# Performance work log

Hardware: AMD Instinct MI355X
Metric: run time of the kernel (lower is better)

Reference implementation:

```python
import jax, jax.numpy as jnp
import numpy as np

B, N, DIM = 4, 2048, 1024
H, DH = 16, 64
SCALE = DH ** -0.5


def setup_inputs() -> dict:
    key = jax.random.key(0)
    k1, k2, k3, k4 = jax.random.split(key, 4)
    x = jax.random.normal(k1, (B, N, DIM), dtype=jnp.float32)
    mask = jax.random.randint(k2, (B, N, N), 0, 2, dtype=jnp.int32)
    W_qkv = jax.random.normal(k3, (DIM, 3 * H * DH), dtype=jnp.float32) * (DIM ** -0.5)
    W_out = jax.random.normal(k4, (H * DH, DIM), dtype=jnp.float32) * ((H * DH) ** -0.5)
    b_out = jnp.zeros((DIM,), dtype=jnp.float32)
    return {"x": x, "mask": mask, "W_qkv": W_qkv, "W_out": W_out, "b_out": b_out}


def reference(x, mask, W_qkv, W_out, b_out):
    # QKV projection: [b, n, 3*h*d]
    qkv = x @ W_qkv
    q, k, v = jnp.split(qkv, 3, axis=-1)
    # 'b n (h d) -> b h n d'
    def to_heads(t):
        b, n, _ = t.shape
        return t.reshape(b, n, H, DH).transpose(0, 2, 1, 3)
    q, k, v = to_heads(q), to_heads(k), to_heads(v)
    # scaled dot-product scores: [b, h, n, n]
    scores = jnp.einsum('bhnd,bhmd->bhnm', q, k) * SCALE
    scores = jnp.where(mask[:, None, :, :] == 1, -jnp.inf, scores)
    att = jax.nn.softmax(scores, axis=-1)
    out = jnp.einsum('bhnm,bhmd->bhnd', att, v)
    # 'b h n d -> b n (h d)'
    out = out.transpose(0, 2, 1, 3).reshape(x.shape[0], x.shape[1], H * DH)
    return out @ W_out + b_out
```

## Files before the change

kernel.cpp:

```cpp
#include <hip/hip_runtime.h>
#include <hip/hip_bf16.h>


typedef __attribute__((ext_vector_type(8))) short bf16x8;
typedef __attribute__((ext_vector_type(4))) float f32x4;

__device__ __forceinline__ unsigned short f2bf(float f) {
  unsigned u = __builtin_bit_cast(unsigned, f);
  u += 0x7fffu + ((u >> 16) & 1u);
  return (unsigned short)(u >> 16);
}

__device__ __forceinline__ void gload16(const void* g, void* l) {
  __builtin_amdgcn_global_load_lds(
      (const __attribute__((address_space(1))) unsigned int*)g,
      (__attribute__((address_space(3))) unsigned int*)l, 16, 0, 0);
}

__device__ __forceinline__ bf16x8 ldsw(const short* base, int row, int elem) {
  const char* p = (const char*)base + row * 128 + ((elem * 2) ^ ((row & 7) << 4));
  return *(const bf16x8*)p;
}

__global__ __launch_bounds__(256) void k_cvt(const float* __restrict__ in,
                                             unsigned short* __restrict__ out) {
  int i = (blockIdx.x * 256 + threadIdx.x) * 4;
  float4 v = *reinterpret_cast<const float4*>(in + i);
  ushort4 o;
  o.x = f2bf(v.x); o.y = f2bf(v.y); o.z = f2bf(v.z); o.w = f2bf(v.w);
  *reinterpret_cast<ushort4*>(out + i) = o;
}

__global__ __launch_bounds__(256) void k_transpose_cvt(const float* __restrict__ in,
                                                       unsigned short* __restrict__ out,
                                                       int rows, int cols) {
  __shared__ float tile[32][33];
  int tx = threadIdx.x & 31, ty = threadIdx.x >> 5;
  int c0 = blockIdx.x * 32, r0 = blockIdx.y * 32;
#pragma unroll
  for (int i = 0; i < 32; i += 8)
    tile[ty + i][tx] = in[(size_t)(r0 + ty + i) * cols + (c0 + tx)];
  __syncthreads();
#pragma unroll
  for (int i = 0; i < 32; i += 8)
    out[(size_t)(c0 + ty + i) * rows + (r0 + tx)] = f2bf(tile[tx][ty + i]);
}

__global__ __launch_bounds__(256) void k_packmask(const int* __restrict__ mask,
                                                  unsigned long long* __restrict__ pack) {
  const int row = blockIdx.x;
  const int t = threadIdx.x, w = t >> 6, lane = t & 63;
  const int* mrow = mask + (size_t)row * 2048;
#pragma unroll
  for (int it = 0; it < 8; ++it) {
    int key = it * 256 + w * 64 + lane;
    unsigned long long bal = __ballot(mrow[key] == 1);
    if (lane == 0) pack[(size_t)row * 32 + it * 4 + w] = bal;
  }
}

template <int EPI>
__global__ __launch_bounds__(256) void k_gemm(
    const unsigned short* __restrict__ A, const unsigned short* __restrict__ Bt,
    unsigned short* __restrict__ Qo, unsigned short* __restrict__ Ko,
    unsigned short* __restrict__ Vo, float* __restrict__ Co,
    const float* __restrict__ bias) {
  __shared__ __align__(16) short Smem[16896];
  short* As = Smem;
  short* Bs = Smem + 8192;
  const int t = threadIdx.x;
  const int NBN = (EPI == 0) ? 24 : 8;
  const int orig = blockIdx.y * NBN + blockIdx.x;
  const int wgid = (orig & 7) * (NBN * 8) + (orig >> 3);
  const int bn = wgid % NBN, bm = wgid / NBN;
  const int wid = t >> 6, lane = t & 63, g = lane >> 4, l15 = lane & 15;
  const int wr = wid >> 1, wc = wid & 1;
  f32x4 zero = {0.f, 0.f, 0.f, 0.f};
  f32x4 acc[4][4];
#pragma unroll
  for (int i = 0; i < 4; ++i)
#pragma unroll
    for (int j = 0; j < 4; ++j) acc[i][j] = zero;

  const char* Ab = (const char*)(A + (size_t)bm * 128 * 1024);
  const char* Bb = (const char*)(Bt + (size_t)bn * 128 * 1024);

  for (int k0 = 0; k0 < 2048; k0 += 128) {
#pragma unroll
    for (int q = 0; q < 4; ++q) {
      int idx = t + q * 256, r = idx >> 3, c = idx & 7;
      int sw = (c * 16) ^ ((r & 7) << 4);
      gload16(Ab + (size_t)r * 2048 + k0 + sw, (char*)As + idx * 16);
      gload16(Bb + (size_t)r * 2048 + k0 + sw, (char*)Bs + idx * 16);
    }
    asm volatile("s_waitcnt vmcnt(0)" ::: "memory");
    __syncthreads();
#pragma unroll
    for (int ks = 0; ks < 2; ++ks) {
      bf16x8 a[4], b[4];
#pragma unroll
      for (int mi = 0; mi < 4; ++mi) a[mi] = ldsw(As, wr * 64 + mi * 16 + l15, ks * 32 + g * 8);
#pragma unroll
      for (int ni = 0; ni < 4; ++ni) b[ni] = ldsw(Bs, wc * 64 + ni * 16 + l15, ks * 32 + g * 8);
#pragma unroll
      for (int mi = 0; mi < 4; ++mi)
#pragma unroll
        for (int ni = 0; ni < 4; ++ni)
          acc[mi][ni] = __builtin_amdgcn_mfma_f32_16x16x32_bf16(a[mi], b[ni], acc[mi][ni], 0, 0, 0);
    }
    __syncthreads();
  }

  if (EPI == 1) {
#pragma unroll
    for (int mi = 0; mi < 4; ++mi)
#pragma unroll
      for (int ni = 0; ni < 4; ++ni)
#pragma unroll
        for (int j = 0; j < 4; ++j) {
          int row = bm * 128 + wr * 64 + mi * 16 + g * 4 + j;
          int col = bn * 128 + wc * 64 + ni * 16 + l15;
          Co[(size_t)row * 1024 + col] = acc[mi][ni][j] + bias[col];
        }
    return;
  }

  const int s = bn >> 3;
  const int h0 = (bn & 7) * 2;
  const int bglob = (bm * 128) >> 11;
  const int n0 = (bm * 128) & 2047;

  if (s < 2) {
    const float qs = (s == 0) ? 0.18033688011112042f : 1.0f;
#pragma unroll
    for (int mi = 0; mi < 4; ++mi)
#pragma unroll
      for (int ni = 0; ni < 4; ++ni)
#pragma unroll
        for (int j = 0; j < 4; ++j)
          Smem[(wr * 64 + mi * 16 + g * 4 + j) * 132 + wc * 64 + ni * 16 + l15] =
              (short)f2bf(acc[mi][ni][j] * qs);
    __syncthreads();
    int r = t >> 1, hh = t & 1;
    unsigned short* dst = (s == 0 ? Qo : Ko) +
        (((size_t)(bglob * 16 + h0 + hh)) * 2048 + n0 + r) * 64;
    const short* src = Smem + r * 132 + hh * 64;
#pragma unroll
    for (int k = 0; k < 8; ++k) {
      uint2 a = *reinterpret_cast<const uint2*>(src + k * 8);
      uint2 b2 = *reinterpret_cast<const uint2*>(src + k * 8 + 4);
      uint4 w = {a.x, a.y, b2.x, b2.y};
      *reinterpret_cast<uint4*>(dst + k * 8) = w;
    }
  } else {
#pragma unroll
    for (int mi = 0; mi < 4; ++mi)
#pragma unroll
      for (int ni = 0; ni < 4; ++ni) {
        unsigned x0 = f2bf(acc[mi][ni][0]), x1 = f2bf(acc[mi][ni][1]);
        unsigned x2 = f2bf(acc[mi][ni][2]), x3 = f2bf(acc[mi][ni][3]);
        uint2 pk = {x0 | (x1 << 16), x2 | (x3 << 16)};
        int col = wc * 64 + ni * 16 + l15;
        int row = wr * 64 + mi * 16 + g * 4;
        *reinterpret_cast<uint2*>(Smem + col * 132 + row) = pk;
      }
    __syncthreads();
    int c = t >> 1, seg = t & 1;
    int h = h0 + (c >> 6), d = c & 63;
    unsigned short* dst = Vo + ((size_t)(bglob * 16 + h) * 64 + d) * 2048 + n0 + seg * 64;
    const short* src = Smem + c * 132 + seg * 64;
#pragma unroll
    for (int k = 0; k < 8; ++k) {
      uint2 a = *reinterpret_cast<const uint2*>(src + k * 8);
      uint2 b2 = *reinterpret_cast<const uint2*>(src + k * 8 + 4);
      uint4 w = {a.x, a.y, b2.x, b2.y};
      *reinterpret_cast<uint4*>(dst + k * 8) = w;
    }
  }
}

__global__ __launch_bounds__(512, 8) void k_attn(
    const unsigned short* __restrict__ Q, const unsigned short* __restrict__ K,
    const unsigned short* __restrict__ Vt_g, const unsigned long long* __restrict__ pack,
    unsigned short* __restrict__ O) {
  __shared__ __align__(16) short Ks[2][64 * 64];
  __shared__ __align__(16) short Vt[2][64 * 64];
  __shared__ __align__(16) short Ps[8][16 * 32];
  const int bid0 = blockIdx.x;
  const int bid = (bid0 & 7) * 128 + (bid0 >> 3);
  const int qt = bid & 15, bh = bid >> 4;
  const int b = bh >> 4;
  const int t = threadIdx.x, wid = t >> 6, lane = t & 63, g = lane >> 4, l15 = lane & 15;
  const char* Kb = (const char*)(K + (size_t)bh * (2048 * 64));
  const char* Vb = (const char*)(Vt_g + (size_t)bh * (64 * 2048));
  const unsigned short* Qb = Q + (size_t)bh * (2048 * 64);

  const int sr = t >> 3, sc = t & 7;
  const int sw_src = (sc * 16) ^ ((sr & 7) << 4);
  char* PwB = (char*)&Ps[wid][0];
  const int ps_rd  = (l15 * 64 + g * 16) ^ ((l15 & 7) << 4);
  const int ps_wr0 = (l15 * 64 + g * 8) ^ ((l15 & 7) << 4);

  gload16(Kb + (size_t)sr * 128 + sw_src, (char*)&Ks[0][0] + t * 16);
  gload16(Vb + (size_t)sr * 4096 + sw_src, (char*)&Vt[0][0] + t * 16);
  const int qrow = qt * 128 + wid * 16 + l15;
  bf16x8 qf0 = *reinterpret_cast<const bf16x8*>(Qb + (size_t)qrow * 64 + g * 8);
  bf16x8 qf1 = *reinterpret_cast<const bf16x8*>(Qb + (size_t)qrow * 64 + 32 + g * 8);
  const unsigned long long* mrow = pack + ((size_t)b * 2048 + qrow) * 32;
  asm volatile("s_waitcnt vmcnt(0)" ::: "memory");
  __syncthreads();

  f32x4 zero = {0.f, 0.f, 0.f, 0.f};
  f32x4 oacc[4];
#pragma unroll
  for (int nf = 0; nf < 4; ++nf) oacc[nf] = zero;
  float lp = 0.f;

  int cb = 0;
#pragma unroll 1
  for (int kt = 0; kt < 32; ++kt) {
    const int nb = cb ^ 1;
    unsigned long long mw = mrow[kt];
    if (kt + 1 < 32) {
      gload16(Kb + (size_t)((kt + 1) * 64 + sr) * 128 + sw_src, (char*)&Ks[nb][0] + t * 16);
      gload16(Vb + (size_t)sr * 4096 + (kt + 1) * 128 + sw_src, (char*)&Vt[nb][0] + t * 16);
    }
    unsigned mlo = (unsigned)mw >> (g * 4);
    unsigned mhi = (unsigned)(mw >> 32) >> (g * 4);
#pragma unroll
    for (int kh = 0; kh < 2; ++kh) {
      f32x4 sf[2] = {zero, zero};
      __builtin_amdgcn_s_setprio(1);
#pragma unroll
      for (int ds = 0; ds < 2; ++ds) {
        bf16x8 qk = ds ? qf1 : qf0;
#pragma unroll
        for (int nf2 = 0; nf2 < 2; ++nf2) {
          bf16x8 kk = ldsw(&Ks[cb][0], (kh * 2 + nf2) * 16 + l15, ds * 32 + g * 8);
          sf[nf2] = __builtin_amdgcn_mfma_f32_16x16x32_bf16(kk, qk, sf[nf2], 0, 0, 0);
        }
      }
      __builtin_amdgcn_s_setprio(0);
      unsigned msrc = kh ? mhi : mlo;
#pragma unroll
      for (int nf2 = 0; nf2 < 2; ++nf2) {
        unsigned eu[4];
#pragma unroll
        for (int j = 0; j < 4; ++j) {
          float s = sf[nf2][j];
          if (msrc & (1u << (nf2 * 16 + j))) s = -1e30f;
          float e = __builtin_amdgcn_exp2f(s);
          lp += e;
          eu[j] = __builtin_bit_cast(unsigned, e);
        }
        uint2 pk;
        pk.x = __builtin_amdgcn_perm(eu[1], eu[0], 0x07060302);
        pk.y = __builtin_amdgcn_perm(eu[3], eu[2], 0x07060302);
        *reinterpret_cast<uint2*>(PwB + (nf2 ? (ps_wr0 ^ 32) : ps_wr0)) = pk;
      }
      asm volatile("s_waitcnt lgkmcnt(0)" ::: "memory");
      __builtin_amdgcn_sched_barrier(0);
      bf16x8 ap = *reinterpret_cast<const bf16x8*>(PwB + ps_rd);
      __builtin_amdgcn_s_setprio(1);
#pragma unroll
      for (int nf = 0; nf < 4; ++nf) {
        bf16x8 bv = ldsw(&Vt[cb][0], nf * 16 + l15, kh * 32 + g * 8);
        oacc[nf] = __builtin_amdgcn_mfma_f32_16x16x32_bf16(ap, bv, oacc[nf], 0, 0, 0);
      }
      __builtin_amdgcn_s_setprio(0);
    }
    asm volatile("s_waitcnt vmcnt(0)" ::: "memory");
    __syncthreads();
    cb = nb;
  }

  float l = lp;
  l += __shfl_xor(l, 16);
  l += __shfl_xor(l, 32);
  float invl = 1.0f / l;
  float inv[4];
#pragma unroll
  for (int j = 0; j < 4; ++j) inv[j] = __shfl(invl, g * 4 + j);

  const int h = bh & 15;
#pragma unroll
  for (int nf = 0; nf < 4; ++nf) {
#pragma unroll
    for (int j = 0; j < 4; ++j) {
      int qg = qt * 128 + wid * 16 + g * 4 + j;
      int d = nf * 16 + l15;
      O[((size_t)b * 2048 + qg) * 1024 + h * 64 + d] = f2bf(oacc[nf][j] * inv[j]);
    }
  }
}

extern "C" void kernel_launch(void* const* d_in, const int* in_sizes, int n_in,
                              void* d_out, int out_size, void* d_ws, size_t ws_size,
                              hipStream_t stream) {
  (void)in_sizes; (void)n_in; (void)out_size; (void)ws_size;
  const float* x = (const float*)d_in[0];
  const int* mask = (const int*)d_in[1];
  const float* Wqkv = (const float*)d_in[2];
  const float* Wout = (const float*)d_in[3];
  const float* bout = (const float*)d_in[4];
  float* out = (float*)d_out;

  unsigned short* ws = (unsigned short*)d_ws;
  unsigned short* Xb   = ws;
  unsigned short* Wq_t = Xb + 8388608;
  unsigned short* Wo_t = Wq_t + 3145728;
  unsigned short* Qa   = Wo_t + 1048576;
  unsigned short* Ka   = Qa + 8388608;
  unsigned short* Va   = Ka + 8388608;
  unsigned short* ATT  = Va + 8388608;
  unsigned long long* MP = (unsigned long long*)(ATT + 8388608);

  k_cvt<<<8192, 256, 0, stream>>>(x, Xb);
  k_transpose_cvt<<<dim3(96, 32), 256, 0, stream>>>(Wqkv, Wq_t, 1024, 3072);
  k_transpose_cvt<<<dim3(32, 32), 256, 0, stream>>>(Wout, Wo_t, 1024, 1024);
  k_packmask<<<8192, 256, 0, stream>>>(mask, MP);
  k_gemm<0><<<dim3(24, 64), 256, 0, stream>>>(Xb, Wq_t, Qa, Ka, Va, nullptr, nullptr);
  k_attn<<<1024, 512, 0, stream>>>(Qa, Ka, Va, MP, ATT);
  k_gemm<1><<<dim3(8, 64), 256, 0, stream>>>(ATT, Wo_t, nullptr, nullptr, nullptr, out, bout);
}
```

Before: 250.5 us.

## Use 32x32x16 MFMA in attention with permlane32 swap instead of LDS P staging

Attention now runs 4 waves of 256 threads per block, each wave owning 32 query rows, and uses 32x32x16 bf16 MFMAs for both QK^T and PV. The score tile is repacked into the PV A-operand layout with permlane32_swap, which removes the per-wave LDS round trip and its waitcnt. The GEMM's grouped block-index swizzle is also removed in favor of plain blockIdx mapping. Each block has fewer waves and more registers per thread, which could lower latency hiding, and dropping the swizzle may hurt L2 locality in the GEMMs.

```diff
diff --git a/kernel.cpp b/kernel.cpp
--- a/kernel.cpp
+++ b/kernel.cpp
@@ -4,6 +4,8 @@
 
 typedef __attribute__((ext_vector_type(8))) short bf16x8;
 typedef __attribute__((ext_vector_type(4))) float f32x4;
+typedef __attribute__((ext_vector_type(16))) float f32x16;
+typedef __attribute__((ext_vector_type(2))) unsigned int uint2v;
 
 __device__ __forceinline__ unsigned short f2bf(float f) {
   unsigned u = __builtin_bit_cast(unsigned, f);
@@ -69,10 +71,7 @@
   short* As = Smem;
   short* Bs = Smem + 8192;
   const int t = threadIdx.x;
-  const int NBN = (EPI == 0) ? 24 : 8;
-  const int orig = blockIdx.y * NBN + blockIdx.x;
-  const int wgid = (orig & 7) * (NBN * 8) + (orig >> 3);
-  const int bn = wgid % NBN, bm = wgid / NBN;
+  const int bn = blockIdx.x, bm = blockIdx.y;
   const int wid = t >> 6, lane = t & 63, g = lane >> 4, l15 = lane & 15;
   const int wr = wid >> 1, wc = wid & 1;
   f32x4 zero = {0.f, 0.f, 0.f, 0.f};
@@ -179,41 +178,45 @@
   }
 }
 
-__global__ __launch_bounds__(512, 8) void k_attn(
+__global__ __launch_bounds__(256) void k_attn(
     const unsigned short* __restrict__ Q, const unsigned short* __restrict__ K,
     const unsigned short* __restrict__ Vt_g, const unsigned long long* __restrict__ pack,
     unsigned short* __restrict__ O) {
   __shared__ __align__(16) short Ks[2][64 * 64];
   __shared__ __align__(16) short Vt[2][64 * 64];
-  __shared__ __align__(16) short Ps[8][16 * 32];
   const int bid0 = blockIdx.x;
   const int bid = (bid0 & 7) * 128 + (bid0 >> 3);
   const int qt = bid & 15, bh = bid >> 4;
   const int b = bh >> 4;
-  const int t = threadIdx.x, wid = t >> 6, lane = t & 63, g = lane >> 4, l15 = lane & 15;
+  const int t = threadIdx.x, wid = t >> 6, lane = t & 63;
+  const int l31 = lane & 31, hi = lane >> 5;
   const char* Kb = (const char*)(K + (size_t)bh * (2048 * 64));
   const char* Vb = (const char*)(Vt_g + (size_t)bh * (64 * 2048));
   const unsigned short* Qb = Q + (size_t)bh * (2048 * 64);
 
-  const int sr = t >> 3, sc = t & 7;
-  const int sw_src = (sc * 16) ^ ((sr & 7) << 4);
-  char* PwB = (char*)&Ps[wid][0];
-  const int ps_rd  = (l15 * 64 + g * 16) ^ ((l15 & 7) << 4);
-  const int ps_wr0 = (l15 * 64 + g * 8) ^ ((l15 & 7) << 4);
-
-  gload16(Kb + (size_t)sr * 128 + sw_src, (char*)&Ks[0][0] + t * 16);
-  gload16(Vb + (size_t)sr * 4096 + sw_src, (char*)&Vt[0][0] + t * 16);
-  const int qrow = qt * 128 + wid * 16 + l15;
-  bf16x8 qf0 = *reinterpret_cast<const bf16x8*>(Qb + (size_t)qrow * 64 + g * 8);
-  bf16x8 qf1 = *reinterpret_cast<const bf16x8*>(Qb + (size_t)qrow * 64 + 32 + g * 8);
+  const int i0 = t, i1 = t + 256;
+  const int r0s = i0 >> 3, r1s = i1 >> 3, cs = (t & 7) * 16;
+  const int k0off = r0s * 128 + (cs ^ ((r0s & 7) << 4));
+  const int k1off = r1s * 128 + (cs ^ ((r1s & 7) << 4));
+  const int v0off = r0s * 4096 + (cs ^ ((r0s & 7) << 4));
+  const int v1off = r1s * 4096 + (cs ^ ((r1s & 7) << 4));
+
+  gload16(Kb + k0off, (char*)&Ks[0][0] + i0 * 16);
+  gload16(Kb + k1off, (char*)&Ks[0][0] + i1 * 16);
+  gload16(Vb + v0off, (char*)&Vt[0][0] + i0 * 16);
+  gload16(Vb + v1off, (char*)&Vt[0][0] + i1 * 16);
+
+  const int qrow = qt * 128 + wid * 32 + l31;
+  bf16x8 qf[4];
+#pragma unroll
+  for (int c = 0; c < 4; ++c)
+    qf[c] = *reinterpret_cast<const bf16x8*>(Qb + (size_t)qrow * 64 + c * 16 + hi * 8);
   const unsigned long long* mrow = pack + ((size_t)b * 2048 + qrow) * 32;
   asm volatile("s_waitcnt vmcnt(0)" ::: "memory");
   __syncthreads();
 
-  f32x4 zero = {0.f, 0.f, 0.f, 0.f};
-  f32x4 oacc[4];
-#pragma unroll
-  for (int nf = 0; nf < 4; ++nf) oacc[nf] = zero;
+  f32x16 oacc0 = {0.f,0.f,0.f,0.f,0.f,0.f,0.f,0.f,0.f,0.f,0.f,0.f,0.f,0.f,0.f,0.f};
+  f32x16 oacc1 = {0.f,0.f,0.f,0.f,0.f,0.f,0.f,0.f,0.f,0.f,0.f,0.f,0.f,0.f,0.f,0.f};
   float lp = 0.f;
 
   int cb = 0;
@@ -222,50 +225,55 @@
     const int nb = cb ^ 1;
     unsigned long long mw = mrow[kt];
     if (kt + 1 < 32) {
-      gload16(Kb + (size_t)((kt + 1) * 64 + sr) * 128 + sw_src, (char*)&Ks[nb][0] + t * 16);
-      gload16(Vb + (size_t)sr * 4096 + (kt + 1) * 128 + sw_src, (char*)&Vt[nb][0] + t * 16);
-    }
-    unsigned mlo = (unsigned)mw >> (g * 4);
-    unsigned mhi = (unsigned)(mw >> 32) >> (g * 4);
+      gload16(Kb + (kt + 1) * 8192 + k0off, (char*)&Ks[nb][0] + i0 * 16);
+      gload16(Kb + (kt + 1) * 8192 + k1off, (char*)&Ks[nb][0] + i1 * 16);
+      gload16(Vb + (kt + 1) * 128 + v0off, (char*)&Vt[nb][0] + i0 * 16);
+      gload16(Vb + (kt + 1) * 128 + v1off, (char*)&Vt[nb][0] + i1 * 16);
+    }
 #pragma unroll
     for (int kh = 0; kh < 2; ++kh) {
-      f32x4 sf[2] = {zero, zero};
+      unsigned m32 = (unsigned)(kh ? (mw >> 32) : mw) >> (4 * hi);
+      f32x16 sf = {0.f,0.f,0.f,0.f,0.f,0.f,0.f,0.f,0.f,0.f,0.f,0.f,0.f,0.f,0.f,0.f};
       __builtin_amdgcn_s_setprio(1);
 #pragma unroll
-      for (int ds = 0; ds < 2; ++ds) {
-        bf16x8 qk = ds ? qf1 : qf0;
-#pragma unroll
-        for (int nf2 = 0; nf2 < 2; ++nf2) {
-          bf16x8 kk = ldsw(&Ks[cb][0], (kh * 2 + nf2) * 16 + l15, ds * 32 + g * 8);
-          sf[nf2] = __builtin_amdgcn_mfma_f32_16x16x32_bf16(kk, qk, sf[nf2], 0, 0, 0);
-        }
+      for (int c = 0; c < 4; ++c) {
+        bf16x8 kk = ldsw(&Ks[cb][0], kh * 32 + l31, c * 16 + hi * 8);
+        sf = __builtin_amdgcn_mfma_f32_32x32x16_bf16(kk, qf[c], sf, 0, 0, 0);
       }
       __builtin_amdgcn_s_setprio(0);
-      unsigned msrc = kh ? mhi : mlo;
-#pragma unroll
-      for (int nf2 = 0; nf2 < 2; ++nf2) {
-        unsigned eu[4];
-#pragma unroll
-        for (int j = 0; j < 4; ++j) {
-          float s = sf[nf2][j];
-          if (msrc & (1u << (nf2 * 16 + j))) s = -1e30f;
-          float e = __builtin_amdgcn_exp2f(s);
-          lp += e;
-          eu[j] = __builtin_bit_cast(unsigned, e);
-        }
-        uint2 pk;
-        pk.x = __builtin_amdgcn_perm(eu[1], eu[0], 0x07060302);
-        pk.y = __builtin_amdgcn_perm(eu[3], eu[2], 0x07060302);
-        *reinterpret_cast<uint2*>(PwB + (nf2 ? (ps_wr0 ^ 32) : ps_wr0)) = pk;
+      unsigned pk[8];
+#pragma unroll
+      for (int p = 0; p < 8; ++p) {
+        const int r0 = 2 * p, r1 = 2 * p + 1;
+        const int b0 = (r0 & 3) + 8 * (r0 >> 2);
+        const int b1 = (r1 & 3) + 8 * (r1 >> 2);
+        float s0 = sf[r0]; if (m32 & (1u << b0)) s0 = -1e30f;
+        float s1 = sf[r1]; if (m32 & (1u << b1)) s1 = -1e30f;
+        float e0 = __builtin_amdgcn_exp2f(s0);
+        float e1 = __builtin_amdgcn_exp2f(s1);
+        lp += e0 + e1;
+        pk[p] = __builtin_amdgcn_perm(__builtin_bit_cast(unsigned, e1),
+                                      __builtin_bit_cast(unsigned, e0), 0x07060302);
       }
-      asm volatile("s_waitcnt lgkmcnt(0)" ::: "memory");
-      __builtin_amdgcn_sched_barrier(0);
-      bf16x8 ap = *reinterpret_cast<const bf16x8*>(PwB + ps_rd);
+      uint2v ra = __builtin_amdgcn_permlane32_swap(pk[0], pk[2], false, false);
+      uint2v rb = __builtin_amdgcn_permlane32_swap(pk[1], pk[3], false, false);
+      uint2v rc = __builtin_amdgcn_permlane32_swap(pk[4], pk[6], false, false);
+      uint2v rd = __builtin_amdgcn_permlane32_swap(pk[5], pk[7], false, false);
+      int4 ia = {(int)ra[0], (int)rb[0], (int)ra[1], (int)rb[1]};
+      int4 ib = {(int)rc[0], (int)rd[0], (int)rc[1], (int)rd[1]};
+      bf16x8 apA = __builtin_bit_cast(bf16x8, ia);
+      bf16x8 apB = __builtin_bit_cast(bf16x8, ib);
       __builtin_amdgcn_s_setprio(1);
-#pragma unroll
-      for (int nf = 0; nf < 4; ++nf) {
-        bf16x8 bv = ldsw(&Vt[cb][0], nf * 16 + l15, kh * 32 + g * 8);
-        oacc[nf] = __builtin_amdgcn_mfma_f32_16x16x32_bf16(ap, bv, oacc[nf], 0, 0, 0);
+      {
+        bf16x8 bv;
+        bv = ldsw(&Vt[cb][0], l31, kh * 32 + hi * 8);
+        oacc0 = __builtin_amdgcn_mfma_f32_32x32x16_bf16(apA, bv, oacc0, 0, 0, 0);
+        bv = ldsw(&Vt[cb][0], l31, kh * 32 + 16 + hi * 8);
+        oacc0 = __builtin_amdgcn_mfma_f32_32x32x16_bf16(apB, bv, oacc0, 0, 0, 0);
+        bv = ldsw(&Vt[cb][0], 32 + l31, kh * 32 + hi * 8);
+        oacc1 = __builtin_amdgcn_mfma_f32_32x32x16_bf16(apA, bv, oacc1, 0, 0, 0);
+        bv = ldsw(&Vt[cb][0], 32 + l31, kh * 32 + 16 + hi * 8);
+        oacc1 = __builtin_amdgcn_mfma_f32_32x32x16_bf16(apB, bv, oacc1, 0, 0, 0);
       }
       __builtin_amdgcn_s_setprio(0);
     }
@@ -274,23 +282,17 @@
     cb = nb;
   }
 
-  float l = lp;
-  l += __shfl_xor(l, 16);
-  l += __shfl_xor(l, 32);
-  float invl = 1.0f / l;
-  float inv[4];
-#pragma unroll
-  for (int j = 0; j < 4; ++j) inv[j] = __shfl(invl, g * 4 + j);
-
+  lp += __shfl_xor(lp, 32);
+  float invl = 1.0f / lp;
   const int h = bh & 15;
 #pragma unroll
-  for (int nf = 0; nf < 4; ++nf) {
-#pragma unroll
-    for (int j = 0; j < 4; ++j) {
-      int qg = qt * 128 + wid * 16 + g * 4 + j;
-      int d = nf * 16 + l15;
-      O[((size_t)b * 2048 + qg) * 1024 + h * 64 + d] = f2bf(oacc[nf][j] * inv[j]);
-    }
+  for (int r = 0; r < 16; ++r) {
+    const int qc = (r & 3) + 8 * (r >> 2);
+    float invr = __shfl(invl, qc + 4 * hi);
+    int qg = qt * 128 + wid * 32 + qc + 4 * hi;
+    size_t base = ((size_t)b * 2048 + qg) * 1024 + h * 64 + l31;
+    O[base] = f2bf(oacc0[r] * invr);
+    O[base + 32] = f2bf(oacc1[r] * invr);
   }
 }
 
@@ -320,6 +322,6 @@
   k_transpose_cvt<<<dim3(32, 32), 256, 0, stream>>>(Wout, Wo_t, 1024, 1024);
   k_packmask<<<8192, 256, 0, stream>>>(mask, MP);
   k_gemm<0><<<dim3(24, 64), 256, 0, stream>>>(Xb, Wq_t, Qa, Ka, Va, nullptr, nullptr);
-  k_attn<<<1024, 512, 0, stream>>>(Qa, Ka, Va, MP, ATT);
+  k_attn<<<1024, 256, 0, stream>>>(Qa, Ka, Va, MP, ATT);
   k_gemm<1><<<dim3(8, 64), 256, 0, stream>>>(ATT, Wo_t, nullptr, nullptr, nullptr, out, bout);
 }
```

Result: no change. 251.0 us (+0.2%).
